# Kernel tuning notes

Hardware: AMD Instinct MI355X
Metric: run time of the kernel (lower is better)

## Reference

```python
import jax, jax.numpy as jnp
import numpy as np
from jax import lax

B, C, H, W, T = 1, 32, 256, 256, 10
Q = 0.2  # dropout prob; keep prob = 0.8


def conv2d(x, w, b=None, pad=0):
    out = lax.conv_general_dilated(x, w, (1, 1), [(pad, pad), (pad, pad)],
                                   dimension_numbers=('NCHW', 'OIHW', 'NCHW'))
    if b is not None:
        out = out + b[None, :, None, None]
    return out


def lrelu(v):
    return jnp.where(v > 0, v, 0.2 * v)


def setup_inputs() -> dict:
    key = jax.random.key(0)
    ks = iter(jax.random.split(key, 80))
    def rn(shape, s=0.05):
        return jax.random.normal(next(ks), shape, jnp.float32) * s
    d = {}
    d['F_1'] = jax.random.normal(next(ks), (B, C, H, W), jnp.float32)
    d['ms'] = jax.random.normal(next(ks), (B, 4, H, W), jnp.float32)
    d['pan'] = jax.random.normal(next(ks), (B, C, H, W), jnp.float32)
    d['masks_u'] = jax.random.uniform(next(ks), (T, 2 * C), jnp.float32)
    # UncertaintyEstimation params
    d['ue_conv_w'] = rn((2 * C, C, 3, 3)); d['ue_conv_b'] = rn((2 * C,), 0.01)
    d['ue_out_w'] = rn((4, 2 * C, 1, 1)); d['ue_out_b'] = rn((4,), 0.01)
    d['ue_aue_w'] = rn((4, 2 * C, 3, 3)); d['ue_aue_b'] = rn((4,), 0.01)
    # UAFM 1x1 convs
    d['conv1_w'] = rn((C, C, 1, 1)); d['conv1_b'] = rn((C,), 0.01)
    d['conv2_w'] = rn((C, C, 1, 1)); d['conv2_b'] = rn((C,), 0.01)
    # two UAConvs (condition_channels=4, channels_in=2C, channels_out=C, k=3)
    for i in (1, 2):
        d[f'spa{i}_w0'] = rn((9, 4, 3, 3)); d[f'spa{i}_b0'] = rn((9,), 0.01)
        d[f'spa{i}_w1'] = rn((9, 9, 1, 1)); d[f'spa{i}_b1'] = rn((9,), 0.01)
        d[f'spa{i}_w2'] = rn((9, 9, 1, 1)); d[f'spa{i}_b2'] = rn((9,), 0.01)
        d[f'spe{i}_w0'] = rn((2 * C, 4, 1, 1)); d[f'spe{i}_b0'] = rn((2 * C,), 0.01)
        d[f'spe{i}_w1'] = rn((2 * C, 2 * C, 1, 1)); d[f'spe{i}_b1'] = rn((2 * C,), 0.01)
        d[f'spe{i}_w2'] = rn((2 * C, 2 * C, 1, 1)); d[f'spe{i}_b2'] = rn((2 * C,), 0.01)
        d[f'ua{i}_w'] = rn((C, 2 * C, 3, 3))
    return d


def uaconv(x, U, sw0, sb0, sw1, sb1, sw2, sb2, pw0, pb0, pw1, pb1, pw2, pb2, Wk):
    # content-adaptive conv: per-pixel spatial (k*k) and spectral (n) attention
    b, n, h, w = x.shape
    a = jax.nn.relu(conv2d(U, sw0, sb0, 1))
    a = jax.nn.relu(conv2d(a, sw1, sb1, 0))
    spat = jax.nn.sigmoid(conv2d(a, sw2, sb2, 0))          # [B, 9, H, W]
    s = jax.nn.relu(conv2d(U, pw0, pb0, 0))
    s = jax.nn.relu(conv2d(s, pw1, pb1, 0))
    spec = jax.nn.sigmoid(conv2d(s, pw2, pb2, 0))          # [B, n, H, W]
    # unfold: patches channel order (c, kh, kw), matching F.unfold
    patches = lax.conv_general_dilated_patches(x, (3, 3), (1, 1), [(1, 1), (1, 1)])
    patches = patches.reshape(b, n, 9, h, w)               # [B, n, 9, H, W]
    rw = patches * spec[:, :, None] * spat[:, None]        # reweight
    Wr = Wk.reshape(Wk.shape[0], n, 9)                     # [m, n, 9]
    return jnp.einsum('bnkhw,mnk->bmhw', rw, Wr)           # fold(k=1) == reshape


def reference(F_1, ms, pan, masks_u,
              ue_conv_w, ue_conv_b, ue_out_w, ue_out_b, ue_aue_w, ue_aue_b,
              conv1_w, conv1_b, conv2_w, conv2_b,
              spa1_w0, spa1_b0, spa1_w1, spa1_b1, spa1_w2, spa1_b2,
              spe1_w0, spe1_b0, spe1_w1, spe1_b1, spe1_w2, spe1_b2, ua1_w,
              spa2_w0, spa2_b0, spa2_w1, spa2_b1, spa2_w2, spa2_b2,
              spe2_w0, spe2_b0, spe2_w1, spe2_b1, spe2_w2, spe2_b2, ua2_w):
    # --- UncertaintyEstimation ---
    x = conv2d(F_1, ue_conv_w, ue_conv_b, 1)               # [B, 2C, H, W]
    mask = (masks_u < (1.0 - Q)).astype(x.dtype)           # [T, 2C] Bernoulli(0.8)
    w4 = ue_out_w[:, :, 0, 0]                              # 1x1 conv as matmul
    # T masked passes, vectorized: xs [T, B, 4, H, W]
    xs = jnp.tanh(jnp.einsum('tc,oc,bchw->tbohw', mask, w4, x)
                  + ue_out_b[None, None, :, None, None]) + ms[None]
    EU = jnp.var(xs, axis=0, ddof=1)                       # unbiased over T
    mean = jnp.mean(xs, axis=0)
    AU = jax.nn.sigmoid(conv2d(x, ue_aue_w, ue_aue_b, 1))
    # --- UAFM ---
    y1 = uaconv(jnp.concatenate([F_1, pan], axis=1), EU,
                spa1_w0, spa1_b0, spa1_w1, spa1_b1, spa1_w2, spa1_b2,
                spe1_w0, spe1_b0, spe1_w1, spe1_b1, spe1_w2, spe1_b2, ua1_w)
    F_2 = lrelu(conv2d(y1, conv1_w, conv1_b, 0))
    y2 = uaconv(jnp.concatenate([F_1, F_2], axis=1), 1.0 - EU,
                spa2_w0, spa2_b0, spa2_w1, spa2_b1, spa2_w2, spa2_b2,
                spe2_w0, spe2_b0, spe2_w1, spe2_b1, spe2_w2, spe2_b2, ua2_w)
    F_out = lrelu(conv2d(y2, conv2_w, conv2_b, 0))
    return (AU, EU, mean, F_out)
```

## Files before the change

kernel.cpp:

```cpp
#include <hip/hip_runtime.h>
#include <hip/hip_bf16.h>
#include <math.h>
#include <string.h>

#define P 65536
#define HH 256
#define WW 256

typedef __attribute__((ext_vector_type(8))) short bf16x8;
typedef __attribute__((ext_vector_type(4))) float f32x4;

__device__ __forceinline__ float fast_sigmoid(float v) {
    return 1.f / (1.f + __expf(-v));
}
__device__ __forceinline__ float fast_tanh(float a) {
    a = fminf(fmaxf(a, -10.f), 10.f);
    float t = __expf(2.f * a);
    return (t - 1.f) / (t + 1.f);
}
__device__ __forceinline__ ushort f2bf(float f) {
    unsigned u = __float_as_uint(f);
    unsigned r = (u + 0x7fffu + ((u >> 16) & 1u)) >> 16;
    return (ushort)r;
}
__device__ __forceinline__ unsigned pack_bf2(float a, float b) {
    __hip_bfloat162 h = __float22bfloat162_rn(make_float2(a, b));
    unsigned u;
    memcpy(&u, &h, 4);
    return u;
}

__global__ __launch_bounds__(256) void setup_k(
        const float* __restrict__ F1, const float* __restrict__ pan,
        ushort* __restrict__ xbf, ushort* __restrict__ panbf,
        const float* __restrict__ ue_w, const float* __restrict__ aue_w,
        const float* __restrict__ ua1, const float* __restrict__ ua2,
        const float* __restrict__ s1w1, const float* __restrict__ s1w2,
        const float* __restrict__ s2w1, const float* __restrict__ s2w2,
        const float* __restrict__ cw1, const float* __restrict__ cw2,
        const float* __restrict__ masks_u, const float* __restrict__ w4,
        float* __restrict__ W, ushort* __restrict__ wub) {
    const int b = blockIdx.x;
    if (b < 512) {
        int idx = b * 256 + threadIdx.x;
        const float* src = (idx < P) ? F1 : pan;
        ushort* dst = (idx < P) ? xbf : panbf;
        int p = idx & (P - 1);
        unsigned pk[16];
        #pragma unroll
        for (int c = 0; c < 16; ++c) {
            float a = src[(2 * c) * P + p];
            float bb = src[(2 * c + 1) * P + p];
            pk[c] = (unsigned)f2bf(a) | ((unsigned)f2bf(bb) << 16);
        }
        uint4* d4 = (uint4*)(dst + (size_t)p * 32);
        #pragma unroll
        for (int q = 0; q < 4; ++q)
            d4[q] = make_uint4(pk[4 * q], pk[4 * q + 1], pk[4 * q + 2], pk[4 * q + 3]);
        return;
    }
    int i = (b - 512) * 256 + threadIdx.x;
    if (i < 2304) {
        int ci = i / 36, r = i % 36, k = r >> 2, co = r & 3;
        W[i] = aue_w[co * 576 + ci * 9 + k];
    } else if (i < 6400) {
        int j = i - 2304;  W[i] = s1w1[(j & 63) * 64 + (j >> 6)];
    } else if (i < 10496) {
        int j = i - 6400;  W[i] = s1w2[(j & 63) * 64 + (j >> 6)];
    } else if (i < 14592) {
        int j = i - 10496; W[i] = s2w1[(j & 63) * 64 + (j >> 6)];
    } else if (i < 18688) {
        int j = i - 14592; W[i] = s2w2[(j & 63) * 64 + (j >> 6)];
    } else if (i < 21248) {
        int j = i - 18688;
        int t = j >> 8, o = (j >> 6) & 3, c = j & 63;
        W[i] = (masks_u[t * 64 + c] < 0.8f) ? w4[o * 64 + c] : 0.f;
    } else if (i < 39680) {
        int j = i - 21248;
        int ct = j / 4608, r1 = j % 4608;
        int kp = r1 / 512, r2 = r1 % 512;
        int n = r2 >> 5, ci = r2 & 31;
        wub[j] = f2bf(ue_w[(ct * 16 + n) * 288 + ci * 9 + kp]);
    } else if (i < 58112) {
        int j = i - 39680;
        int mo = j / 576, K = j % 576, k = K >> 6, n = K & 63;
        float s = 0.f;
        for (int m = 0; m < 32; ++m)
            s += cw1[mo * 32 + m] * ua1[m * 576 + n * 9 + k];
        wub[18432 + j] = f2bf(s);
    } else if (i < 76544) {
        int j = i - 58112;
        int mo = j / 576, K = j % 576, k = K >> 6, n = K & 63;
        float s = 0.f;
        for (int m = 0; m < 32; ++m)
            s += cw2[mo * 32 + m] * ua2[m * 576 + n * 9 + k];
        wub[36864 + j] = f2bf(s);
    }
}

__global__ __launch_bounds__(256) void conv_ue_mfma(
        const ushort* __restrict__ xbf, const ushort* __restrict__ wbfu,
        const float* __restrict__ bias, ushort* __restrict__ xnh) {
    __shared__ float tls[4][272];
    const int tid  = threadIdx.x;
    const int lane = tid & 63;
    const int wv   = __builtin_amdgcn_readfirstlane(tid >> 6);
    const int lrow = lane & 15;
    const int kg   = lane >> 4;

    bf16x8 zf;
    #pragma unroll
    for (int z = 0; z < 8; ++z) zf[z] = 0;

    bf16x8 Bf[9];
    const ushort* wb = wbfu + wv * 4608;
    #pragma unroll
    for (int kp = 0; kp < 9; ++kp)
        Bf[kp] = *(const bf16x8*)(wb + kp * 512 + lrow * 32 + kg * 8);

    const float bco = bias[wv * 16 + lrow];
    float* tw = tls[wv];

    for (int si = 0; si < 4; ++si) {
        const int s   = blockIdx.x * 4 + si;
        const int row = s >> 4;
        const int cb  = (s & 15) << 4;
        const int pb  = s << 4;
        f32x4 acc = {bco, bco, bco, bco};
        #pragma unroll
        for (int dh = -1; dh <= 1; ++dh) {
            if ((unsigned)(row + dh) >= 256u) continue;
            #pragma unroll
            for (int dw = -1; dw <= 1; ++dw) {
                const bool kill = (dw == -1 && cb == 0 && lrow == 0) ||
                                  (dw == 1 && cb == 240 && lrow == 15);
                const int apx = kill ? pb : (pb + dh * 256 + dw + lrow);
                bf16x8 Af = *(const bf16x8*)(xbf + (size_t)apx * 32 + kg * 8);
                if (kill) Af = zf;
                acc = __builtin_amdgcn_mfma_f32_16x16x32_bf16(
                          Af, Bf[(dh + 1) * 3 + (dw + 1)], acc, 0, 0, 0);
            }
        }
        #pragma unroll
        for (int j = 0; j < 4; ++j)
            tw[(kg * 4 + j) * 17 + lrow] = acc[j];
        asm volatile("s_waitcnt lgkmcnt(0)" ::: "memory");
        {
            const float* rp = tw + lrow * 17;
            unsigned o[8];
            #pragma unroll
            for (int q = 0; q < 8; ++q)
                o[q] = pack_bf2(rp[2 * q], rp[2 * q + 1]);
            ushort* dst = xnh + (size_t)(pb + lrow) * 64 + wv * 16;
            *(uint4*)dst       = make_uint4(o[0], o[1], o[2], o[3]);
            *(uint4*)(dst + 8) = make_uint4(o[4], o[5], o[6], o[7]);
        }
        asm volatile("s_waitcnt lgkmcnt(0)" ::: "memory");
    }
}

__global__ __launch_bounds__(256) void head_k(
        const ushort* __restrict__ xnh, const float* __restrict__ aue_wt,
        const float* __restrict__ aue_b, const float* __restrict__ mw,
        const float* __restrict__ b4, const float* __restrict__ msin,
        float* __restrict__ AU, float* __restrict__ EU, float* __restrict__ MEAN) {
    __shared__ float cs[64][65];
    __shared__ float pr[4][4][64];
    const int tid = threadIdx.x;
    const int pxg = tid & 63;
    const int g   = __builtin_amdgcn_readfirstlane(tid >> 6);
    const int p   = blockIdx.x * 64 + pxg;
    const int h = p >> 8, x0 = p & 255;
    const int cib = g * 16;

    float pa[4] = {0.f, 0.f, 0.f, 0.f};
    float cv[16];
    #pragma unroll
    for (int k = 0; k < 9; ++k) {
        const int dh = k / 3 - 1, dw = k % 3 - 1;
        if ((unsigned)(h + dh) >= 256u) continue;
        const bool kill = (dw == -1 && x0 == 0) || (dw == 1 && x0 == 255);
        const int pxe = kill ? p : (p + dh * 256 + dw);
        const ushort* sp = xnh + (size_t)pxe * 64 + cib;
        uint4 ra = *(const uint4*)sp;
        uint4 rb = *(const uint4*)(sp + 8);
        unsigned rr[8] = {ra.x, ra.y, ra.z, ra.w, rb.x, rb.y, rb.z, rb.w};
        if (kill) {
            #pragma unroll
            for (int q = 0; q < 8; ++q) rr[q] = 0;
        }
        float f[16];
        #pragma unroll
        for (int q = 0; q < 8; ++q) {
            f[2 * q]     = __uint_as_float(rr[q] << 16);
            f[2 * q + 1] = __uint_as_float(rr[q] & 0xffff0000u);
        }
        if (k == 4) {
            #pragma unroll
            for (int ci = 0; ci < 16; ++ci) cv[ci] = f[ci];
        }
        #pragma unroll
        for (int ci = 0; ci < 16; ++ci) {
            const float* wp = aue_wt + (cib + ci) * 36 + k * 4;
            #pragma unroll
            for (int co = 0; co < 4; ++co)
                pa[co] = fmaf(f[ci], wp[co], pa[co]);
        }
    }
    #pragma unroll
    for (int co = 0; co < 4; ++co) pr[co][g][pxg] = pa[co];
    #pragma unroll
    for (int ci = 0; ci < 16; ++ci) cs[pxg][cib + ci] = cv[ci];
    __syncthreads();

    {
        float s = aue_b[g] + pr[g][0][pxg] + pr[g][1][pxg]
                           + pr[g][2][pxg] + pr[g][3][pxg];
        AU[g * P + p] = fast_sigmoid(s);
    }

    float xv[64];
    #pragma unroll
    for (int c = 0; c < 64; ++c) xv[c] = cs[pxg][c];
    float msv = msin[g * P + p];
    float bo  = b4[g];
    float vals[10];
    float s = 0.f;
    #pragma unroll
    for (int t = 0; t < 10; ++t) {
        float a = bo;
        const float* mwp = mw + t * 256 + g * 64;
        #pragma unroll
        for (int c = 0; c < 64; ++c) a = fmaf(mwp[c], xv[c], a);
        float v = fast_tanh(a) + msv;
        vals[t] = v;
        s += v;
    }
    float m = s * 0.1f;
    MEAN[g * P + p] = m;
    float var = 0.f;
    #pragma unroll
    for (int t = 0; t < 10; ++t) { float d = vals[t] - m; var = fmaf(d, d, var); }
    EU[g * P + p] = var * (1.0f / 9.0f);
}

template<int OUTMODE>
__global__ __launch_bounds__(256) void ua_fused_k(
        const float* __restrict__ U, int flip,
        const float* __restrict__ aw0, const float* __restrict__ ab0,
        const float* __restrict__ aw1, const float* __restrict__ ab1,
        const float* __restrict__ aw2, const float* __restrict__ ab2,
        const float* __restrict__ pw0, const float* __restrict__ pb0,
        const float* __restrict__ pw1t, const float* __restrict__ pb1,
        const float* __restrict__ pw2t, const float* __restrict__ pb2,
        const ushort* __restrict__ xa, const ushort* __restrict__ xb,
        const ushort* __restrict__ w2bf, const float* __restrict__ cb,
        float* __restrict__ outf, ushort* __restrict__ outh) {
    __shared__ float sbuf[64 * 64];
    __shared__ unsigned spec_lu[64][40];
    __shared__ float spat_l[9][64];
    const int tid = threadIdx.x;
    const int pxg = tid & 63;
    const int g   = __builtin_amdgcn_readfirstlane(tid >> 6);
    const int cbase = g * 16;
    const int p   = blockIdx.x * 64 + pxg;
    const int h = p >> 8, x0 = p & 255;

    {
        float u[4];
        #pragma unroll
        for (int ci = 0; ci < 4; ++ci) {
            float v = U[ci * P + p];
            u[ci] = flip ? 1.f - v : v;
        }
        float h2[16];
        #pragma unroll
        for (int j = 0; j < 16; ++j) h2[j] = pb1[cbase + j];
        #pragma unroll 8
        for (int ci = 0; ci < 64; ++ci) {
            float s = pb0[ci];
            #pragma unroll
            for (int k = 0; k < 4; ++k) s = fmaf(u[k], pw0[ci * 4 + k], s);
            float hv = fmaxf(s, 0.f);
            const float* wr = pw1t + ci * 64 + cbase;
            #pragma unroll
            for (int j = 0; j < 16; ++j) h2[j] = fmaf(hv, wr[j], h2[j]);
        }
        #pragma unroll
        for (int j = 0; j < 16; ++j)
            sbuf[(cbase + j) * 64 + pxg] = fmaxf(h2[j], 0.f);
        __syncthreads();

        float h3[16];
        #pragma unroll
        for (int j = 0; j < 16; ++j) h3[j] = pb2[cbase + j];
        #pragma unroll 8
        for (int ci = 0; ci < 64; ++ci) {
            float hv = sbuf[ci * 64 + pxg];
            const float* wr = pw2t + ci * 64 + cbase;
            #pragma unroll
            for (int j = 0; j < 16; ++j) h3[j] = fmaf(hv, wr[j], h3[j]);
        }
        #pragma unroll
        for (int q = 0; q < 8; ++q)
            spec_lu[pxg][(cbase >> 1) + q] =
                pack_bf2(fast_sigmoid(h3[2 * q]), fast_sigmoid(h3[2 * q + 1]));

        float uh[4][9];
        #pragma unroll
        for (int ci = 0; ci < 4; ++ci) {
            const float* up = U + ci * P;
            #pragma unroll
            for (int kh = 0; kh < 3; ++kh) {
                int hh = h + kh - 1;
                bool hok = (unsigned)hh < 256u;
                #pragma unroll
                for (int kw = 0; kw < 3; ++kw) {
                    int wx = x0 + kw - 1;
                    bool ok = hok && (unsigned)wx < 256u;
                    float v = ok ? up[hh * WW + wx] : 0.f;
                    if (flip && ok) v = 1.f - v;
                    uh[ci][kh * 3 + kw] = v;
                }
            }
        }
        float a1[9];
        #pragma unroll
        for (int co = 0; co < 9; ++co) {
            float s = ab0[co];
            #pragma unroll
            for (int ci = 0; ci < 4; ++ci)
                #pragma unroll
                for (int k = 0; k < 9; ++k)
                    s = fmaf(uh[ci][k], aw0[co * 36 + ci * 9 + k], s);
            a1[co] = fmaxf(s, 0.f);
        }
        float a2[9];
        #pragma unroll
        for (int co = 0; co < 9; ++co) {
            float s = ab1[co];
            #pragma unroll
            for (int ci = 0; ci < 9; ++ci) s = fmaf(a1[ci], aw1[co * 9 + ci], s);
            a2[co] = fmaxf(s, 0.f);
        }
        #pragma unroll
        for (int cq = 0; cq < 3; ++cq) {
            const int co = g + cq * 4;
            if (co < 9) {
                float s = ab2[co];
                #pragma unroll
                for (int ci = 0; ci < 9; ++ci) s = fmaf(a2[ci], aw2[co * 9 + ci], s);
                spat_l[co][pxg] = fast_sigmoid(s);
            }
        }
    }
    __syncthreads();

    const int lane = tid & 63;
    const int lrow = lane & 15;
    const int kg   = lane >> 4;
    const int wv   = g;
    const int s    = blockIdx.x * 4 + wv;
    const int row  = s >> 4;
    const int c16  = s & 15;
    const int pb   = s << 4;
    const int px   = pb + lrow;
    const int pxl  = wv * 16 + lrow;

    float sl[8], sh[8];
    {
        const unsigned* sp = &spec_lu[pxl][kg * 4];
        #pragma unroll
        for (int q = 0; q < 4; ++q) {
            unsigned uu = sp[q];
            sl[2 * q]     = __uint_as_float(uu << 16);
            sl[2 * q + 1] = __uint_as_float(uu & 0xffff0000u);
        }
        const unsigned* sp2 = &spec_lu[pxl][16 + kg * 4];
        #pragma unroll
        for (int q = 0; q < 4; ++q) {
            unsigned uu = sp2[q];
            sh[2 * q]     = __uint_as_float(uu << 16);
            sh[2 * q + 1] = __uint_as_float(uu & 0xffff0000u);
        }
    }
    const ushort* b0p = w2bf + lrow * 576 + kg * 8;
    const ushort* b1p = w2bf + (16 + lrow) * 576 + kg * 8;

    f32x4 acc0 = {0.f, 0.f, 0.f, 0.f};
    f32x4 acc1 = {0.f, 0.f, 0.f, 0.f};

    #pragma unroll
    for (int k = 0; k < 9; ++k) {
        const int dh = k / 3 - 1, dw = k % 3 - 1;
        if ((unsigned)(row + dh) >= 256u) continue;
        const bool kill = (dw == -1 && c16 == 0 && lrow == 0) ||
                          (dw == 1 && c16 == 15 && lrow == 15);
        float stk = spat_l[k][pxl];
        if (kill) stk = 0.f;
        const int pxe = kill ? px : (px + dh * 256 + dw);
        #pragma unroll
        for (int par = 0; par < 2; ++par) {
            const ushort* src = (par == 0) ? (xa + (size_t)pxe * 32 + kg * 8)
                                           : (xb + (size_t)pxe * 32 + kg * 8);
            uint4 raw = *(const uint4*)src;
            const float* ss = par ? sh : sl;
            unsigned rr[4] = {raw.x, raw.y, raw.z, raw.w};
            union { unsigned u[4]; bf16x8 v; } af;
            #pragma unroll
            for (int q = 0; q < 4; ++q) {
                float e0 = __uint_as_float(rr[q] << 16)          * (ss[2 * q] * stk);
                float e1 = __uint_as_float(rr[q] & 0xffff0000u)  * (ss[2 * q + 1] * stk);
                af.u[q] = pack_bf2(e0, e1);
            }
            const int ki = k * 2 + par;
            bf16x8 bf0 = *(const bf16x8*)(b0p + ki * 32);
            bf16x8 bf1 = *(const bf16x8*)(b1p + ki * 32);
            acc0 = __builtin_amdgcn_mfma_f32_16x16x32_bf16(af.v, bf0, acc0, 0, 0, 0);
            acc1 = __builtin_amdgcn_mfma_f32_16x16x32_bf16(af.v, bf1, acc1, 0, 0, 0);
        }
    }

    const float cb0 = cb[lrow], cb1 = cb[16 + lrow];
    float* tw = sbuf + wv * 560;
    #pragma unroll
    for (int j = 0; j < 4; ++j) {
        float y0 = acc0[j] + cb0; y0 = y0 > 0.f ? y0 : 0.2f * y0;
        float y1 = acc1[j] + cb1; y1 = y1 > 0.f ? y1 : 0.2f * y1;
        tw[(kg * 4 + j) * 35 + lrow] = y0;
        tw[(kg * 4 + j) * 35 + 16 + lrow] = y1;
    }
    asm volatile("s_waitcnt lgkmcnt(0)" ::: "memory");
    if constexpr (OUTMODE == 0) {
        const float* rp = tw + lrow * 35 + kg * 8;
        unsigned o[4];
        #pragma unroll
        for (int q = 0; q < 4; ++q)
            o[q] = pack_bf2(rp[2 * q], rp[2 * q + 1]);
        *(uint4*)(outh + (size_t)(pb + lrow) * 32 + kg * 8) =
            make_uint4(o[0], o[1], o[2], o[3]);
    } else {
        #pragma unroll
        for (int it = 0; it < 8; ++it) {
            const int mo = kg * 8 + it;
            outf[mo * P + pb + lrow] = tw[lrow * 35 + mo];
        }
    }
    asm volatile("s_waitcnt lgkmcnt(0)" ::: "memory");
}

extern "C" void kernel_launch(void* const* d_in, const int* in_sizes, int n_in,
                              void* d_out, int out_size, void* d_ws, size_t ws_size,
                              hipStream_t stream) {
    const float* F1        = (const float*)d_in[0];
    const float* ms        = (const float*)d_in[1];
    const float* pan       = (const float*)d_in[2];
    const float* masks_u   = (const float*)d_in[3];
    const float* ue_conv_w = (const float*)d_in[4];
    const float* ue_conv_b = (const float*)d_in[5];
    const float* ue_out_w  = (const float*)d_in[6];
    const float* ue_out_b  = (const float*)d_in[7];
    const float* ue_aue_w  = (const float*)d_in[8];
    const float* ue_aue_b  = (const float*)d_in[9];
    const float* conv1_w   = (const float*)d_in[10];
    const float* conv1_b   = (const float*)d_in[11];
    const float* conv2_w   = (const float*)d_in[12];
    const float* conv2_b   = (const float*)d_in[13];
    const float* spa1_w0 = (const float*)d_in[14];
    const float* spa1_b0 = (const float*)d_in[15];
    const float* spa1_w1 = (const float*)d_in[16];
    const float* spa1_b1 = (const float*)d_in[17];
    const float* spa1_w2 = (const float*)d_in[18];
    const float* spa1_b2 = (const float*)d_in[19];
    const float* spe1_w0 = (const float*)d_in[20];
    const float* spe1_b0 = (const float*)d_in[21];
    const float* spe1_w1 = (const float*)d_in[22];
    const float* spe1_b1 = (const float*)d_in[23];
    const float* spe1_w2 = (const float*)d_in[24];
    const float* spe1_b2 = (const float*)d_in[25];
    const float* ua1_w   = (const float*)d_in[26];
    const float* spa2_w0 = (const float*)d_in[27];
    const float* spa2_b0 = (const float*)d_in[28];
    const float* spa2_w1 = (const float*)d_in[29];
    const float* spa2_b1 = (const float*)d_in[30];
    const float* spa2_w2 = (const float*)d_in[31];
    const float* spa2_b2 = (const float*)d_in[32];
    const float* spe2_w0 = (const float*)d_in[33];
    const float* spe2_b0 = (const float*)d_in[34];
    const float* spe2_w1 = (const float*)d_in[35];
    const float* spe2_b1 = (const float*)d_in[36];
    const float* spe2_w2 = (const float*)d_in[37];
    const float* spe2_b2 = (const float*)d_in[38];
    const float* ua2_w   = (const float*)d_in[39];

    float* out  = (float*)d_out;
    float* AU   = out;
    float* EU   = out + 4 * P;
    float* MEAN = out + 8 * P;
    float* FOUT = out + 12 * P;

    float* ws    = (float*)d_ws;
    ushort* xbf   = (ushort*)ws;
    ushort* panbf = (ushort*)(ws + 16 * P);
    ushort* xnh   = (ushort*)(ws + 32 * P);
    ushort* f2nh  = (ushort*)(ws + 64 * P);
    float* W     = ws + 80 * P;
    float* aue_wt = W;
    float* s1w1t  = W + 2304;
    float* s1w2t  = W + 6400;
    float* s2w1t  = W + 10496;
    float* s2w2t  = W + 14592;
    float* mw     = W + 18688;
    ushort* wub   = (ushort*)(W + 21248);
    ushort* wbfu  = wub;
    ushort* w2bf1 = wub + 18432;
    ushort* w2bf2 = wub + 36864;

    dim3 blk(256);

    setup_k<<<dim3(812), blk, 0, stream>>>(F1, pan, xbf, panbf,
                                           ue_conv_w, ue_aue_w, ua1_w, ua2_w,
                                           spe1_w1, spe1_w2, spe2_w1, spe2_w2,
                                           conv1_w, conv2_w, masks_u, ue_out_w, W, wub);

    conv_ue_mfma<<<dim3(1024), blk, 0, stream>>>(xbf, wbfu, ue_conv_b, xnh);
    head_k<<<dim3(1024), blk, 0, stream>>>(xnh, aue_wt, ue_aue_b, mw, ue_out_b, ms,
                                           AU, EU, MEAN);

    ua_fused_k<0><<<dim3(1024), blk, 0, stream>>>(
        EU, 0,
        spa1_w0, spa1_b0, spa1_w1, spa1_b1, spa1_w2, spa1_b2,
        spe1_w0, spe1_b0, s1w1t, spe1_b1, s1w2t, spe1_b2,
        xbf, panbf, w2bf1, conv1_b, nullptr, f2nh);

    ua_fused_k<1><<<dim3(1024), blk, 0, stream>>>(
        EU, 1,
        spa2_w0, spa2_b0, spa2_w1, spa2_b1, spa2_w2, spa2_b2,
        spe2_w0, spe2_b0, s2w1t, spe2_b1, s2w2t, spe2_b2,
        xbf, f2nh, w2bf2, conv2_b, FOUT, nullptr);
}
```

Baseline: 133.4 us.

## Compute spectral attention 64x64 layers with bf16 MFMA instead of scalar FMA

The two 64x64 spectral-attention 1x1 layers inside the fused UA kernel move from per-thread fp32 FMA loops to bf16 MFMA 16x16x32, using ping/pong LDS tiles of bf16 activations. Weights are pre-packed into MFMA fragment layout in the setup kernel and held in registers, and the old transposed fp32 weight copies are removed. The aim is to cut the VALU cost of the spectral MLP, in exchange for reduced precision on those activations, extra register pressure from the weight fragments, and reuse of the ping/pong buffers by later stages.

```diff
diff --git a/kernel.cpp b/kernel.cpp
--- a/kernel.cpp
+++ b/kernel.cpp
@@ -63,14 +63,7 @@
     if (i < 2304) {
         int ci = i / 36, r = i % 36, k = r >> 2, co = r & 3;
         W[i] = aue_w[co * 576 + ci * 9 + k];
-    } else if (i < 6400) {
-        int j = i - 2304;  W[i] = s1w1[(j & 63) * 64 + (j >> 6)];
-    } else if (i < 10496) {
-        int j = i - 6400;  W[i] = s1w2[(j & 63) * 64 + (j >> 6)];
-    } else if (i < 14592) {
-        int j = i - 10496; W[i] = s2w1[(j & 63) * 64 + (j >> 6)];
     } else if (i < 18688) {
-        int j = i - 14592; W[i] = s2w2[(j & 63) * 64 + (j >> 6)];
     } else if (i < 21248) {
         int j = i - 18688;
         int t = j >> 8, o = (j >> 6) & 3, c = j & 63;
@@ -95,6 +88,14 @@
         for (int m = 0; m < 32; ++m)
             s += cw2[mo * 32 + m] * ua2[m * 576 + n * 9 + k];
         wub[36864 + j] = f2bf(s);
+    } else if (i < 92928) {
+        int j = i - 76544;
+        int mat = j >> 12;
+        int r = j & 4095;
+        int ct = r >> 10, kk = (r >> 9) & 1, n = (r >> 5) & 15, c = r & 31;
+        const float* src = (mat == 0) ? s1w1 : (mat == 1) ? s1w2
+                         : (mat == 2) ? s2w1 : s2w2;
+        wub[55296 + j] = f2bf(src[(ct * 16 + n) * 64 + kk * 32 + c]);
     }
 }
 
@@ -251,20 +252,33 @@
         const float* __restrict__ aw1, const float* __restrict__ ab1,
         const float* __restrict__ aw2, const float* __restrict__ ab2,
         const float* __restrict__ pw0, const float* __restrict__ pb0,
-        const float* __restrict__ pw1t, const float* __restrict__ pb1,
-        const float* __restrict__ pw2t, const float* __restrict__ pb2,
+        const float* __restrict__ pb1, const float* __restrict__ pb2,
+        const ushort* __restrict__ wspe,
         const ushort* __restrict__ xa, const ushort* __restrict__ xb,
         const ushort* __restrict__ w2bf, const float* __restrict__ cb,
         float* __restrict__ outf, ushort* __restrict__ outh) {
-    __shared__ float sbuf[64 * 64];
-    __shared__ unsigned spec_lu[64][40];
+    __shared__ __align__(16) ushort ping[64 * 72];
+    __shared__ __align__(16) ushort pong[64 * 72];
     __shared__ float spat_l[9][64];
     const int tid = threadIdx.x;
     const int pxg = tid & 63;
     const int g   = __builtin_amdgcn_readfirstlane(tid >> 6);
-    const int cbase = g * 16;
+    const int cib = g * 16;
     const int p   = blockIdx.x * 64 + pxg;
     const int h = p >> 8, x0 = p & 255;
+    const int lane = tid & 63;
+    const int lrow = lane & 15;
+    const int kg   = lane >> 4;
+
+    bf16x8 Wf[2][4][2];
+    #pragma unroll
+    for (int ly = 0; ly < 2; ++ly)
+        #pragma unroll
+        for (int ct = 0; ct < 4; ++ct)
+            #pragma unroll
+            for (int kk = 0; kk < 2; ++kk)
+                Wf[ly][ct][kk] = *(const bf16x8*)(wspe + ly * 4096 +
+                                     ct * 1024 + kk * 512 + lrow * 32 + kg * 8);
 
     {
         float u[4];
@@ -273,39 +287,51 @@
             float v = U[ci * P + p];
             u[ci] = flip ? 1.f - v : v;
         }
-        float h2[16];
-        #pragma unroll
-        for (int j = 0; j < 16; ++j) h2[j] = pb1[cbase + j];
-        #pragma unroll 8
-        for (int ci = 0; ci < 64; ++ci) {
-            float s = pb0[ci];
-            #pragma unroll
-            for (int k = 0; k < 4; ++k) s = fmaf(u[k], pw0[ci * 4 + k], s);
-            float hv = fmaxf(s, 0.f);
-            const float* wr = pw1t + ci * 64 + cbase;
-            #pragma unroll
-            for (int j = 0; j < 16; ++j) h2[j] = fmaf(hv, wr[j], h2[j]);
-        }
-        #pragma unroll
-        for (int j = 0; j < 16; ++j)
-            sbuf[(cbase + j) * 64 + pxg] = fmaxf(h2[j], 0.f);
-        __syncthreads();
-
-        float h3[16];
-        #pragma unroll
-        for (int j = 0; j < 16; ++j) h3[j] = pb2[cbase + j];
-        #pragma unroll 8
-        for (int ci = 0; ci < 64; ++ci) {
-            float hv = sbuf[ci * 64 + pxg];
-            const float* wr = pw2t + ci * 64 + cbase;
-            #pragma unroll
-            for (int j = 0; j < 16; ++j) h3[j] = fmaf(hv, wr[j], h3[j]);
-        }
-        #pragma unroll
-        for (int q = 0; q < 8; ++q)
-            spec_lu[pxg][(cbase >> 1) + q] =
-                pack_bf2(fast_sigmoid(h3[2 * q]), fast_sigmoid(h3[2 * q + 1]));
-
+        unsigned* prow = (unsigned*)ping + (pxg * 72 + cib) / 2;
+        #pragma unroll
+        for (int cl = 0; cl < 8; ++cl) {
+            int c0 = cib + 2 * cl, c1 = c0 + 1;
+            float s0 = pb0[c0], s1 = pb0[c1];
+            #pragma unroll
+            for (int k = 0; k < 4; ++k) {
+                s0 = fmaf(u[k], pw0[c0 * 4 + k], s0);
+                s1 = fmaf(u[k], pw0[c1 * 4 + k], s1);
+            }
+            prow[cl] = pack_bf2(fmaxf(s0, 0.f), fmaxf(s1, 0.f));
+        }
+    }
+    __syncthreads();
+
+    #pragma unroll
+    for (int ct = 0; ct < 4; ++ct) {
+        f32x4 a = {0.f, 0.f, 0.f, 0.f};
+        #pragma unroll
+        for (int kk = 0; kk < 2; ++kk) {
+            bf16x8 A = *(const bf16x8*)&ping[(g * 16 + lrow) * 72 + kk * 32 + kg * 8];
+            a = __builtin_amdgcn_mfma_f32_16x16x32_bf16(A, Wf[0][ct][kk], a, 0, 0, 0);
+        }
+        float b = pb1[ct * 16 + lrow];
+        #pragma unroll
+        for (int j = 0; j < 4; ++j)
+            pong[(g * 16 + kg * 4 + j) * 72 + ct * 16 + lrow] = f2bf(fmaxf(a[j] + b, 0.f));
+    }
+    asm volatile("s_waitcnt lgkmcnt(0)" ::: "memory");
+    #pragma unroll
+    for (int ct = 0; ct < 4; ++ct) {
+        f32x4 a = {0.f, 0.f, 0.f, 0.f};
+        #pragma unroll
+        for (int kk = 0; kk < 2; ++kk) {
+            bf16x8 A = *(const bf16x8*)&pong[(g * 16 + lrow) * 72 + kk * 32 + kg * 8];
+            a = __builtin_amdgcn_mfma_f32_16x16x32_bf16(A, Wf[1][ct][kk], a, 0, 0, 0);
+        }
+        float b = pb2[ct * 16 + lrow];
+        #pragma unroll
+        for (int j = 0; j < 4; ++j)
+            ping[(g * 16 + kg * 4 + j) * 72 + ct * 16 + lrow] =
+                f2bf(fast_sigmoid(a[j] + b));
+    }
+
+    {
         float uh[4][9];
         #pragma unroll
         for (int ci = 0; ci < 4; ++ci) {
@@ -356,9 +382,6 @@
     }
     __syncthreads();
 
-    const int lane = tid & 63;
-    const int lrow = lane & 15;
-    const int kg   = lane >> 4;
     const int wv   = g;
     const int s    = blockIdx.x * 4 + wv;
     const int row  = s >> 4;
@@ -369,14 +392,14 @@
 
     float sl[8], sh[8];
     {
-        const unsigned* sp = &spec_lu[pxl][kg * 4];
+        const unsigned* sp = (const unsigned*)&ping[pxl * 72 + kg * 8];
         #pragma unroll
         for (int q = 0; q < 4; ++q) {
             unsigned uu = sp[q];
             sl[2 * q]     = __uint_as_float(uu << 16);
             sl[2 * q + 1] = __uint_as_float(uu & 0xffff0000u);
         }
-        const unsigned* sp2 = &spec_lu[pxl][16 + kg * 4];
+        const unsigned* sp2 = (const unsigned*)&ping[pxl * 72 + 32 + kg * 8];
         #pragma unroll
         for (int q = 0; q < 4; ++q) {
             unsigned uu = sp2[q];
@@ -422,7 +445,7 @@
     }
 
     const float cb0 = cb[lrow], cb1 = cb[16 + lrow];
-    float* tw = sbuf + wv * 560;
+    float* tw = (float*)pong + wv * 560;
     #pragma unroll
     for (int j = 0; j < 4; ++j) {
         float y0 = acc0[j] + cb0; y0 = y0 > 0.f ? y0 : 0.2f * y0;
@@ -506,19 +529,17 @@
     ushort* f2nh  = (ushort*)(ws + 64 * P);
     float* W     = ws + 80 * P;
     float* aue_wt = W;
-    float* s1w1t  = W + 2304;
-    float* s1w2t  = W + 6400;
-    float* s2w1t  = W + 10496;
-    float* s2w2t  = W + 14592;
     float* mw     = W + 18688;
     ushort* wub   = (ushort*)(W + 21248);
     ushort* wbfu  = wub;
     ushort* w2bf1 = wub + 18432;
     ushort* w2bf2 = wub + 36864;
+    ushort* wspe1 = wub + 55296;
+    ushort* wspe2 = wub + 63488;
 
     dim3 blk(256);
 
-    setup_k<<<dim3(812), blk, 0, stream>>>(F1, pan, xbf, panbf,
+    setup_k<<<dim3(875), blk, 0, stream>>>(F1, pan, xbf, panbf,
                                            ue_conv_w, ue_aue_w, ua1_w, ua2_w,
                                            spe1_w1, spe1_w2, spe2_w1, spe2_w2,
                                            conv1_w, conv2_w, masks_u, ue_out_w, W, wub);
@@ -530,12 +551,12 @@
     ua_fused_k<0><<<dim3(1024), blk, 0, stream>>>(
         EU, 0,
         spa1_w0, spa1_b0, spa1_w1, spa1_b1, spa1_w2, spa1_b2,
-        spe1_w0, spe1_b0, s1w1t, spe1_b1, s1w2t, spe1_b2,
+        spe1_w0, spe1_b0, spe1_b1, spe1_b2, wspe1,
         xbf, panbf, w2bf1, conv1_b, nullptr, f2nh);
 
     ua_fused_k<1><<<dim3(1024), blk, 0, stream>>>(
         EU, 1,
         spa2_w0, spa2_b0, spa2_w1, spa2_b1, spa2_w2, spa2_b2,
-        spe2_w0, spe2_b0, s2w1t, spe2_b1, s2w2t, spe2_b2,
+        spe2_w0, spe2_b0, spe2_b1, spe2_b2, wspe2,
         xbf, f2nh, w2bf2, conv2_b, FOUT, nullptr);
 }
```

Measured after the change: 113.7 us. -14.8%, faster.
